# Kernel tuning notes

Hardware: AMD Instinct MI355X
Metric: run time of the kernel (lower is better)

Reference implementation:

```python
import jax, jax.numpy as jnp
import numpy as np

WINDOW = 32


def _dilate(mask, iters=5):
    # scipy binary_dilation with default cross structure, `iters` iterations
    m = mask.copy()
    for _ in range(iters):
        d = m.copy()
        d[1:, :] |= m[:-1, :]
        d[:-1, :] |= m[1:, :]
        d[:, 1:] |= m[:, :-1]
        d[:, :-1] |= m[:, 1:]
        m = d
    return m


def _label8(mask):
    # skimage measure.label, default 8-connectivity, via min-label propagation
    h, w = mask.shape
    lab = np.where(mask, np.arange(1, mask.size + 1, dtype=np.int64).reshape(h, w), 0)
    BIG = mask.size + 2
    while True:
        p = np.pad(np.where(mask, lab, BIG), 1, constant_values=BIG)
        m = np.full((h, w), BIG, dtype=np.int64)
        for dy in (-1, 0, 1):
            for dx in (-1, 0, 1):
                m = np.minimum(m, p[1 + dy:1 + dy + h, 1 + dx:1 + dx + w])
        new = np.where(mask, m, 0)
        if np.array_equal(new, lab):
            break
        lab = new
    u = np.unique(lab)
    out = np.searchsorted(u, lab)
    if u[0] != 0:
        out = out + 1
    return out


def _malis(seg_flat, e1, e2, costs, pos):
    # MALIS edge weights: Kruskal on descending affinities with union-find;
    # pos=True counts same-(nonzero)-label pairs merged by each edge,
    # pos=False counts cross-label pairs between labeled nodes.
    n = seg_flat.size
    parent = np.arange(n)
    cnt = [dict() for _ in range(n)]
    for i in range(n):
        s = int(seg_flat[i])
        if s != 0:
            cnt[i][s] = 1
    w = np.zeros(costs.shape[0], np.float32)

    def find(x):
        r = x
        while parent[r] != r:
            r = parent[r]
        while parent[x] != r:
            parent[x], x = r, parent[x]
        return r

    order = np.argsort(-costs, kind='stable')
    for ei in order:
        ra, rb = find(int(e1[ei])), find(int(e2[ei]))
        if ra == rb:
            continue
        ca, cb = cnt[ra], cnt[rb]
        small, large = (ca, cb) if len(ca) <= len(cb) else (cb, ca)
        same = 0
        for kk, v in small.items():
            same += v * large.get(kk, 0)
        if pos:
            w[ei] = same
        else:
            sa = sum(ca.values())
            sb = sum(cb.values())
            w[ei] = sa * sb - same
        parent[rb] = ra
        for kk, v in cb.items():
            ca[kk] = ca.get(kk, 0) + v
        cnt[rb] = None
    return w


def compute_malis_weights(pred_np, target_np):
    B, C, H, W = pred_np.shape
    wn_full = np.zeros(pred_np.shape, np.float32)
    wp_full = np.zeros(pred_np.shape, np.float32)
    win = WINDOW
    idx = np.arange(win * win).reshape(win, win)
    e1 = np.concatenate([idx[:, :-1].ravel(), idx[:-1, :].ravel()])
    e2 = np.concatenate([idx[:, 1:].ravel(), idx[1:, :].ravel()])
    for k in range(H // win):
        for j in range(W // win):
            p = pred_np[:, :, k * win:(k + 1) * win, j * win:(j + 1) * win]
            t = target_np[:, :, k * win:(k + 1) * win, j * win:(j + 1) * win]
            costs = np.concatenate([
                (p[:, :, :, :-1] + p[:, :, :, 1:]).reshape(B, -1),
                (p[:, :, :-1, :] + p[:, :, 1:, :]).reshape(B, -1)], axis=1).astype(np.float32)
            gtc = np.concatenate([
                (t[:, :, :, :-1] + t[:, :, :, 1:]).reshape(B, -1),
                (t[:, :, :-1, :] + t[:, :, 1:, :]).reshape(B, -1)], axis=1).astype(np.float32)
            costs_n = costs.copy()
            costs_p = costs.copy()
            costs_n[gtc > 20] = 20
            costs_p[gtc < 10] = 0
            gtc = np.minimum(gtc, 20)
            for i in range(B):
                sg = _label8(_dilate(t[i, 0] == 0, 5) == 0)
                en = _malis(sg.ravel(), e1, e2, costs_n[i], False)
                ep = _malis(sg.ravel(), e1, e2, costs_p[i], True)
                sn = en.sum()
                if sn > 0:
                    en = en / sn
                sp = ep.sum()
                if sp > 0:
                    ep = ep / sp
                en[gtc[i] >= 10] = 0
                ep[gtc[i] < 20] = 0
                for ew, out in ((en, wn_full), (ep, wp_full)):
                    wh, wv = np.split(ew, 2)
                    wh = wh.reshape(win, win - 1)
                    wv = wv.reshape(win - 1, win)
                    nodes = np.zeros((win, win), np.float32)
                    nodes[:, :-1] += wh
                    nodes[:, 1:] += wh
                    nodes[:-1, :] += wv
                    nodes[1:, :] += wv
                    out[i, 0, k * win:(k + 1) * win, j * win:(j + 1) * win] = nodes
    return wn_full, wp_full


def setup_inputs() -> dict:
    key = jax.random.key(0)
    k1, k2 = jax.random.split(key)
    pred = jax.random.uniform(k1, (2, 1, 256, 256), jnp.float32) * 20.0
    target = jax.random.randint(k2, (2, 1, 256, 256), 0, 26).astype(jnp.float32)
    return {"pred": pred, "target": target, "malis_lr": 1.0, "malis_lr_pos": 1.0}


def reference(pred, target, malis_lr, malis_lr_pos):
    # weights are computed from detached values (CPU graph algorithm), constants wrt autodiff
    wn, wp = compute_malis_weights(np.asarray(pred), np.asarray(target))
    wn = jnp.asarray(wn, jnp.float32)
    wp = jnp.asarray(wp, jnp.float32)
    loss = malis_lr * jnp.square(pred) * wn + malis_lr_pos * jnp.square(20.0 - pred) * wp
    return loss.sum()
```

## Files before the change

### kernel.cpp

```cpp
#include <hip/hip_runtime.h>
#include <cstdint>

#define NPIX  1024
#define NH    992
#define NEDGE 1984
#define NSORT 2048
#define NGRP  31
#define HFS   4300
#define POOLN (NPIX + 2*HFS)

typedef unsigned long long u64;
typedef unsigned int u32;

static __device__ __forceinline__ u64 packRoot(int sL,int off,int len,int cap){
    return (u64)(u32)(sL & 0x7FF) | ((u64)(u32)(off & 0x3FFF) << 11) |
           ((u64)(u32)(len & 0x7FF) << 25) | ((u64)(u32)(cap & 0x7FF) << 36);
}
#define R_SL(R)  ((int)((R) & 0x7FF))
#define R_OFF(R) ((int)(((R)>>11) & 0x3FFF))
#define R_LEN(R) ((int)(((R)>>25) & 0x7FF))
#define R_CAP(R) ((int)(((R)>>36) & 0x7FF))

static __device__ __forceinline__ int rdl(int v, int l){ return __builtin_amdgcn_readlane(v, l); }

static __device__ __forceinline__ u64 sxor64(u64 v, int m){
    u32 lo = (u32)__shfl_xor((int)(v & 0xFFFFFFFFull), m, 64);
    u32 hi = (u32)__shfl_xor((int)(v >> 32), m, 64);
    return ((u64)hi << 32) | lo;
}

static __device__ __forceinline__ void edgeAB(int e, int &a, int &b){
    if (e < NH) { int r = (int)((unsigned)e / 31u); a = e + r; b = a + 1; }
    else        { a = e - NH; b = a + 32; }
}

#define CE(x, y, up) { u64 _a=(x), _b=(y); bool _lt=(_a<_b); \
    u64 _mn=_lt?_a:_b, _mx=_lt?_b:_a; (x)=(up)?_mn:_mx; (y)=(up)?_mx:_mn; }
#define CEX(x, xm, keepmin) { u64 _p=sxor64((x),(xm)); bool _lt=((x)<_p); \
    u64 _mn=_lt?(x):_p, _mx=_lt?_p:(x); (x)=(keepmin)?_mn:_mx; }

static __device__ __forceinline__ int wredi(int v){
    #pragma unroll
    for (int o = 32; o > 0; o >>= 1) v += __shfl_xor(v, o, 64);
    return v;
}
static __device__ __forceinline__ float wredf(float v){
    #pragma unroll
    for (int o = 32; o > 0; o >>= 1) v += __shfl_xor(v, o, 64);
    return v;
}

__global__ __launch_bounds__(128) void malis_kernel(
    const float* __restrict__ pred,
    const float* __restrict__ target,
    const float* __restrict__ lr_p,
    const float* __restrict__ lrp_p,
    float* __restrict__ out)
{
    const int tid  = threadIdx.x;
    const int lane = tid & 63;
    const int wv   = tid >> 6;
    const int bid  = blockIdx.x;
    const int bb   = bid >> 6;
    const int win  = bid & 63;
    const int wy   = win >> 3, wx = win & 7;
    const int base = bb * 65536 + (wy * 32) * 256 + wx * 32;

    __shared__ __align__(16) u32 Ks[2][NSORT];
    __shared__ u64   root[2][NPIX];
    __shared__ float predL[NPIX];
    __shared__ float costs[NEDGE];
    __shared__ u32   poolS[2][POOLN];
    __shared__ u32   Q[2][NPIX];
    __shared__ float Qw[2][NPIX];
    __shared__ short seg[NPIX];
    __shared__ short par[2][NPIX];
    __shared__ short H[2][NPIX + 1];
    __shared__ unsigned char tgtL[NPIX];
    __shared__ unsigned char gtcL[NEDGE];
    __shared__ u32   rowmaskL[32];
    __shared__ u32   fgL[32];
    __shared__ unsigned short baseL[33];
    __shared__ int   flags[2];

    u32* runPar = (u32*)poolS;
    unsigned short* labIdRun = (unsigned short*)(runPar + 512);

    for (int j = 0; j < 8; ++j) {
        int i = tid + 128 * j;
        int r = i >> 5, c = i & 31;
        float pv = pred[base + r * 256 + c];
        float tv = target[base + r * 256 + c];
        predL[i] = pv;
        tgtL[i]  = (unsigned char)tv;
        u64 zb = __ballot(tv == 0.0f);
        if (lane == 0) {
            int rr = 4 * j + 2 * wv;
            rowmaskL[rr]     = (u32)zb;
            rowmaskL[rr + 1] = (u32)(zb >> 32);
        }
    }
    if (tid == 0) flags[1] = 0;
    for (int x = tid; x < 512; x += 128) runPar[x] = (u32)x;
    __syncthreads();

    if (tid == 0) {
        u32 m0[32];
        #pragma unroll
        for (int r = 0; r < 32; ++r) m0[r] = rowmaskL[r];
        #pragma unroll
        for (int it = 0; it < 5; ++it) {
            u32 d[32];
            #pragma unroll
            for (int r = 0; r < 32; ++r) {
                u32 v = m0[r] | (m0[r] << 1) | (m0[r] >> 1);
                if (r > 0)  v |= m0[r - 1];
                if (r < 31) v |= m0[r + 1];
                d[r] = v;
            }
            #pragma unroll
            for (int r = 0; r < 32; ++r) m0[r] = d[r];
        }
        int acc = 0;
        #pragma unroll
        for (int r = 0; r < 32; ++r) {
            u32 f = ~m0[r];
            fgL[r] = f;
            baseL[r] = (unsigned short)acc;
            acc += __popc(f & ~(f << 1));
        }
        baseL[32] = (unsigned short)acc;
    }
    __syncthreads();
    const int nRuns = (int)baseL[32];

    for (;;) {
        if (tid == 0) flags[0] = 0;
        __syncthreads();
        bool chg = false;
        for (int j = 0; j < 8; ++j) {
            int i = tid + 128 * j;
            int r = i >> 5, c = i & 31;
            if (r == 0) continue;
            u32 fr = fgL[r];
            if (!((fr >> c) & 1u)) continue;
            u32 fu = fgL[r - 1];
            u32 nb = fu & (u32)((7ull << c) >> 1);
            if (!nb) continue;
            u32 Sr = fr & ~(fr << 1);
            int a = (int)baseL[r] + __popc(Sr & ((2u << c) - 1u)) - 1;
            for (;;) { int p = (int)runPar[a]; if (p == a) break; a = p; }
            u32 Su = fu & ~(fu << 1);
            int bu = (int)baseL[r - 1];
            while (nb) {
                int cc = __ffs((int)nb) - 1; nb &= nb - 1;
                int b = bu + __popc(Su & ((2u << cc) - 1u)) - 1;
                for (;;) { int p = (int)runPar[b]; if (p == b) break; b = p; }
                if (a != b) {
                    int mnr = a < b ? a : b;
                    int mxr = a ^ b ^ mnr;
                    atomicMin(&runPar[mxr], (u32)mnr);
                    chg = true;
                    a = mnr;
                }
            }
        }
        if (chg) flags[0] = 1;
        __syncthreads();
        if (!flags[0]) break;
        for (int x = tid; x < nRuns; x += 128) {
            u32 p = runPar[x];
            runPar[x] = runPar[p];
        }
        __syncthreads();
    }

    for (int x = tid; x < nRuns; x += 128)
        if ((int)runPar[x] == x) labIdRun[x] = (unsigned short)atomicAdd(&flags[1], 1);
    __syncthreads();

    for (int j = 0; j < 8; ++j) {
        int i = tid + 128 * j;
        int r = i >> 5, c = i & 31;
        u32 fr = fgL[r];
        short s = 0;
        if ((fr >> c) & 1u) {
            u32 Sr = fr & ~(fr << 1);
            int x = (int)baseL[r] + __popc(Sr & ((2u << c) - 1u)) - 1;
            for (;;) { int p = (int)runPar[x]; if (p == x) break; x = p; }
            s = (short)((int)labIdRun[x] + 1);
        }
        seg[i] = s;
    }

    for (int e = tid; e < NEDGE; e += 128) {
        int a, b2; edgeAB(e, a, b2);
        costs[e] = predL[a] + predL[b2];
        gtcL[e]  = (unsigned char)(tgtL[a] + tgtL[b2]);
    }
    __syncthreads();

    const int ph = wv;
    u32*   Ks_   = Ks[ph];
    short* par_  = par[ph];
    u64*   root_ = root[ph];
    u32*   pool_ = poolS[ph];
    short* H_    = H[ph];
    u32*   Q_    = Q[ph];
    float* Qw_   = Qw[ph];
    u32*   claim_= (u32*)Qw[ph];

    u64 sk[32];
    #pragma unroll
    for (int r = 0; r < 32; ++r) {
        int e = lane * 32 + r;
        u64 kv = ~0ULL;
        if (e < NEDGE) {
            float cv = costs[e];
            int g = gtcL[e];
            if (ph == 0) { if (g > 20) cv = 20.0f; }
            else         { if (g < 10) cv = 0.0f; }
            kv = (((u64)(~__float_as_uint(cv))) << 32) | (u32)e;
        }
        sk[r] = kv;
    }
    #pragma unroll
    for (int kk2 = 2; kk2 <= 32; kk2 <<= 1) {
        #pragma unroll
        for (int j = kk2 >> 1; j > 0; j >>= 1) {
            #pragma unroll
            for (int r = 0; r < 32; ++r) {
                if ((r & j) == 0) {
                    bool up = (kk2 == 32) ? ((lane & 1) == 0) : ((r & kk2) == 0);
                    CE(sk[r], sk[r | j], up);
                }
            }
        }
    }
    #pragma unroll
    for (int kk2 = 64; kk2 <= 2048; kk2 <<= 1) {
        const bool up = ((lane & (kk2 >> 5)) == 0);
        #pragma unroll
        for (int j = kk2 >> 1; j >= 32; j >>= 1) {
            const int xm = j >> 5;
            const bool keepmin = (((lane & xm) == 0) == up);
            #pragma unroll
            for (int r = 0; r < 32; ++r) { CEX(sk[r], xm, keepmin); }
        }
        #pragma unroll
        for (int j = 16; j > 0; j >>= 1) {
            #pragma unroll
            for (int r = 0; r < 32; ++r) {
                if ((r & j) == 0) { CE(sk[r], sk[r | j], up); }
            }
        }
    }
    #pragma unroll
    for (int r = 0; r < 32; r += 4) {
        uint4 v4;
        v4.x = (u32)sk[r]; v4.y = (u32)sk[r+1]; v4.z = (u32)sk[r+2]; v4.w = (u32)sk[r+3];
        *(uint4*)&Ks_[lane * 32 + r] = v4;
    }

    for (int i = lane; i < NPIX; i += 64) {
        short s2 = seg[i];
        par_[i] = (short)(i | (s2 ? 0x8000 : 0));
        if (s2) {
            root_[i] = packRoot(1, i, 1, 1);
            pool_[i] = ((u32)(unsigned short)s2 << 16) | 1u;
        } else {
            root_[i] = 0;
        }
        H_[i] = 0;
        claim_[i] = ~0u;
    }
    if (lane == 0) H_[NPIX] = 0;
    __builtin_amdgcn_wave_barrier();

    int qn = 0;
    u32 rnd = 1;
    const u64 ltm = (1ull << lane) - 1;
    int curE = (int)Ks_[lane];
    for (int g2 = 0; g2 < NGRP; ++g2) {
        int nextE = (g2 + 1 < NGRP) ? (int)Ks_[(g2 + 1) * 64 + lane] : 0;
        const int myE = curE;
        int ea, eb2; edgeAB(myE, ea, eb2);
        int ra = ea, rb = eb2;
        int laA, laB;
        for (;;) {
            int va = (int)(unsigned short)par_[ra];
            int vb = (int)(unsigned short)par_[rb];
            int pa = va & 0x3FF, pb = vb & 0x3FF;
            bool fa = (pa != ra), fb = (pb != rb);
            if (!fa && !fb) { laA = va >> 15; laB = vb >> 15; break; }
            int ga = (int)(unsigned short)par_[pa];
            int gb = (int)(unsigned short)par_[pb];
            if (fa) { par_[ra] = (short)ga; ra = ga & 0x3FF; }
            if (fb) { par_[rb] = (short)gb; rb = gb & 0x3FF; }
        }
        bool alive = (ra != rb);

        for (;;) {
            if (!__ballot(alive)) break;
            const bool av = alive;
            const u32 tag = ((0x03FFFFFFu - rnd) << 6) | (u32)lane;
            ++rnd;
            int mn = ra < rb ? ra : rb;
            int mx = ra < rb ? rb : ra;
            int winner = (laA == laB) ? mn : (laA ? ra : rb);
            int loser  = (laA == laB) ? mx : (laA ? rb : ra);
            bool wgt = (laA & laB) != 0;
            if (av)        atomicMin(&claim_[loser],  tag);
            if (av && wgt) atomicMin(&claim_[winner], tag);
            bool sel = false;
            if (av) {
                u32 cl = claim_[loser];
                u32 cw = wgt ? claim_[winner] : tag;
                sel = (cl == tag) && (cw == tag);
            }
            u64 wm = __ballot(sel && wgt);
            if (sel && wgt) Q_[qn + __popcll(wm & ltm)] =
                (u32)myE | ((u32)mn << 11) | ((u32)mx << 21);
            qn += (int)__popcll(wm);
            if (sel) par_[loser] = (short)winner;
            if (av) {
                for (;;) {
                    int va = (int)(unsigned short)par_[ra];
                    int vb = (int)(unsigned short)par_[rb];
                    int pa = va & 0x3FF, pb = vb & 0x3FF;
                    bool fa = (pa != ra), fb = (pb != rb);
                    if (!fa && !fb) { laA = va >> 15; laB = vb >> 15; break; }
                    int ga = (int)(unsigned short)par_[pa];
                    int gb = (int)(unsigned short)par_[pb];
                    if (fa) { par_[ra] = (short)ga; ra = ga & 0x3FF; }
                    if (fb) { par_[rb] = (short)gb; rb = gb & 0x3FF; }
                }
                alive = !sel && (ra != rb);
            }
        }
        curE = nextE;
        __builtin_amdgcn_wave_barrier();
    }

    u32 bump = NPIX;
    u32 halfEnd = NPIX + HFS;
    int curHalf = 0;

    auto do_gc = [&]() {
        u32 tgt = (curHalf == 0) ? (u32)(NPIX + HFS) : (u32)NPIX;
        u32 nb = tgt;
        for (int c = 0; c < 16; ++c) {
            int i0 = c * 64 + lane;
            bool live = (root_[i0] != 0);
            u64 rbm = __ballot(live);
            while (rbm) {
                int j = __ffsll(rbm) - 1; rbm &= rbm - 1;
                int r = c * 64 + j;
                u64 R = root_[r];
                int len = R_LEN(R);
                int off = R_OFF(R);
                for (int t = lane; t < len; t += 64) {
                    u32 v2 = pool_[off + t];
                    pool_[nb + t] = v2;
                }
                __builtin_amdgcn_wave_barrier();
                if (lane == 0) root_[r] = packRoot(R_SL(R), (int)nb, len, len);
                nb += (u32)len;
            }
        }
        bump = nb;
        halfEnd = tgt + HFS;
        curHalf ^= 1;
    };

    for (int q = 0; q < qn; ++q) {
        u32 rec = Q_[q];
        int A  = (int)((rec >> 11) & 0x3FF);
        int B  = (int)((rec >> 21) & 0x3FF);
        int winner = A;
        int dead   = B;
        u64 RA = root_[A], RB = root_[B];
        int sLa = R_SL(RA), sLb = R_SL(RB);
        int lenA = R_LEN(RA), lenB = R_LEN(RB);
        if (bump + (u32)(lenA + lenB + 8) > halfEnd) {
            do_gc();
            RA = root_[A]; RB = root_[B];
            lenA = R_LEN(RA); lenB = R_LEN(RB);
        }
        int offA = R_OFF(RA), capA = R_CAP(RA);
        int offB = R_OFF(RB), capB = R_CAP(RB);
        int offS, lenS, offL, lenL, capL;
        if (lenA <= lenB) { offS = offA; lenS = lenA; offL = offB; lenL = lenB; capL = capB; }
        else              { offS = offB; lenS = lenB; offL = offA; lenL = lenA; capL = capA; }
        int same = 0, dOff, dLen, dCap;

        if (lenS + lenL <= 64) {
            u32 eL = (lane < lenL) ? pool_[offL + lane] : 0u;
            u32 eS = (lane < lenS) ? pool_[offS + lane] : 0u;
            dLen = lenL;
            for (int t = 0; t < lenS; ++t) {
                u32 xs = (u32)rdl((int)eS, t);
                bool match = (lane < lenL) && ((eL >> 16) == (xs >> 16));
                u64 mb = __ballot(match);
                if (mb) {
                    int ml = __ffsll(mb) - 1;
                    same += (int)(xs & 0xFFFF) * ((int)rdl((int)eL, ml) & 0xFFFF);
                    if (match) eL += (xs & 0xFFFF);
                } else {
                    if (lane == dLen) eL = xs;
                    dLen++;
                }
            }
            if (dLen <= capL) { dOff = offL; dCap = capL; }
            else { dOff = (int)bump; dCap = (dLen + 3) & ~3; bump += (u32)dCap; }
            if (lane < dLen) pool_[dOff + lane] = eL;
        } else {
            dOff = (int)bump;
            dCap = (lenL + lenS + 4) & ~3; bump += (u32)dCap;
            for (int j = lane; j < lenS; j += 64) {
                u32 es = pool_[offS + j];
                H_[es >> 16] = (short)(es & 0xFFFF);
            }
            __builtin_amdgcn_wave_barrier();
            int sp = 0;
            for (int j = lane; j < lenL; j += 64) {
                u32 el = pool_[offL + j];
                int h = (int)H_[el >> 16];
                sp += h * (int)(el & 0xFFFF);
                pool_[dOff + j] = el + (u32)h;
                if (h) H_[el >> 16] = 0;
            }
            same = wredi(sp);
            __builtin_amdgcn_wave_barrier();
            int baseU = 0;
            for (int j0 = 0; j0 < lenS; j0 += 64) {
                int j = j0 + lane;
                bool un = false; u32 es = 0;
                if (j < lenS) { es = pool_[offS + j]; un = (H_[es >> 16] != 0); }
                u64 ub = __ballot(un);
                if (un) {
                    int pos = __popcll(ub & ltm);
                    pool_[dOff + lenL + baseU + pos] = es;
                    H_[es >> 16] = 0;
                }
                baseU += __popcll(ub);
            }
            dLen = lenL + baseU;
        }
        if (lane == 0) {
            Qw_[q] = (float)(ph ? same : (sLa * sLb - same));
            root_[winner] = packRoot(sLa + sLb, dOff, dLen, dCap);
            root_[dead]   = 0;
        }
        __builtin_amdgcn_wave_barrier();
    }

    float s_loc = 0.0f;
    for (int q = lane; q < qn; q += 64) s_loc += Qw_[q];
    const float sn = wredf(s_loc);

    const float scale = ph ? lrp_p[0] : lr_p[0];
    float acc = 0.0f;
    for (int q = lane; q < qn; q += 64) {
        float wv2 = Qw_[q];
        if (wv2 == 0.0f) continue;
        if (sn > 0.0f) wv2 /= sn;
        int me = (int)(Q_[q] & 0x7FF);
        int g = gtcL[me];
        bool zero = ph ? (g < 20) : (g >= 10);
        if (zero) continue;
        int a2, b2; edgeAB(me, a2, b2);
        float pa = predL[a2], pb = predL[b2];
        float fa2, fb2;
        if (ph == 0) { fa2 = pa * pa; fb2 = pb * pb; }
        else { float qa = 20.0f - pa, qb = 20.0f - pb; fa2 = qa * qa; fb2 = qb * qb; }
        acc += scale * wv2 * (fa2 + fb2);
    }
    acc = wredf(acc);
    if (lane == 0) atomicAdd(out, acc);
}

__global__ void zero_out_kernel(float* o)
{
    if (threadIdx.x == 0 && blockIdx.x == 0) o[0] = 0.0f;
}

extern "C" void kernel_launch(void* const* d_in, const int* in_sizes, int n_in,
                              void* d_out, int out_size, void* d_ws, size_t ws_size,
                              hipStream_t stream)
{
    const float* pred   = (const float*)d_in[0];
    const float* target = (const float*)d_in[1];
    const float* lr     = (const float*)d_in[2];
    const float* lrp    = (const float*)d_in[3];
    float* out = (float*)d_out;

    zero_out_kernel<<<1, 64, 0, stream>>>(out);
    malis_kernel<<<128, 128, 0, stream>>>(pred, target, lr, lrp, out);
}
```

Measured before the change: 346.0 us.

## Split monolithic MALIS kernel into seg, sort, drain and replay kernels

Breaks the single 128-block kernel, where each block handled one window and both phases, into four kernels. Segmentation, per-phase sorting, union-find draining and replay now run as separate launches, with intermediates passed through workspace memory. Each of the later three kernels runs 256 single-wave blocks with smaller LDS footprints, aiming at more parallelism and occupancy across CUs. The seg kernel also parallelises the dilation and the prefix sum across 32 lanes using shuffles. In exchange it adds extra launch overhead and global-memory round trips for sorted keys, segments and queues.

```diff
diff --git a/kernel.cpp b/kernel.cpp
--- a/kernel.cpp
+++ b/kernel.cpp
@@ -12,6 +12,11 @@
 typedef unsigned long long u64;
 typedef unsigned int u32;
 
+#define WS_SEG   0
+#define WS_KS    262144
+#define WS_Q     2359296
+#define WS_QN    3407872
+
 static __device__ __forceinline__ u64 packRoot(int sL,int off,int len,int cap){
     return (u64)(u32)(sL & 0x7FF) | ((u64)(u32)(off & 0x3FFF) << 11) |
            ((u64)(u32)(len & 0x7FF) << 25) | ((u64)(u32)(cap & 0x7FF) << 36);
@@ -34,6 +39,13 @@
     else        { a = e - NH; b = a + 32; }
 }
 
+static __device__ __forceinline__ int winBase(int wslot){
+    int bb = wslot >> 6;
+    int win = wslot & 63;
+    int wy = win >> 3, wx = win & 7;
+    return bb * 65536 + (wy * 32) * 256 + wx * 32;
+}
+
 #define CE(x, y, up) { u64 _a=(x), _b=(y); bool _lt=(_a<_b); \
     u64 _mn=_lt?_a:_b, _mx=_lt?_b:_a; (x)=(up)?_mn:_mx; (y)=(up)?_mx:_mn; }
 #define CEX(x, xm, keepmin) { u64 _p=sxor64((x),(xm)); bool _lt=((x)<_p); \
@@ -50,49 +62,27 @@
     return v;
 }
 
-__global__ __launch_bounds__(128) void malis_kernel(
-    const float* __restrict__ pred,
+__global__ __launch_bounds__(128) void seg_kernel(
     const float* __restrict__ target,
-    const float* __restrict__ lr_p,
-    const float* __restrict__ lrp_p,
-    float* __restrict__ out)
+    unsigned short* __restrict__ segW)
 {
     const int tid  = threadIdx.x;
     const int lane = tid & 63;
     const int wv   = tid >> 6;
     const int bid  = blockIdx.x;
-    const int bb   = bid >> 6;
-    const int win  = bid & 63;
-    const int wy   = win >> 3, wx = win & 7;
-    const int base = bb * 65536 + (wy * 32) * 256 + wx * 32;
-
-    __shared__ __align__(16) u32 Ks[2][NSORT];
-    __shared__ u64   root[2][NPIX];
-    __shared__ float predL[NPIX];
-    __shared__ float costs[NEDGE];
-    __shared__ u32   poolS[2][POOLN];
-    __shared__ u32   Q[2][NPIX];
-    __shared__ float Qw[2][NPIX];
-    __shared__ short seg[NPIX];
-    __shared__ short par[2][NPIX];
-    __shared__ short H[2][NPIX + 1];
-    __shared__ unsigned char tgtL[NPIX];
-    __shared__ unsigned char gtcL[NEDGE];
+    const int base = winBase(bid);
+
     __shared__ u32   rowmaskL[32];
     __shared__ u32   fgL[32];
     __shared__ unsigned short baseL[33];
+    __shared__ u32   runPar[512];
+    __shared__ unsigned short labIdRun[512];
     __shared__ int   flags[2];
-
-    u32* runPar = (u32*)poolS;
-    unsigned short* labIdRun = (unsigned short*)(runPar + 512);
 
     for (int j = 0; j < 8; ++j) {
         int i = tid + 128 * j;
         int r = i >> 5, c = i & 31;
-        float pv = pred[base + r * 256 + c];
         float tv = target[base + r * 256 + c];
-        predL[i] = pv;
-        tgtL[i]  = (unsigned char)tv;
         u64 zb = __ballot(tv == 0.0f);
         if (lane == 0) {
             int rr = 4 * j + 2 * wv;
@@ -104,32 +94,27 @@
     for (int x = tid; x < 512; x += 128) runPar[x] = (u32)x;
     __syncthreads();
 
-    if (tid == 0) {
-        u32 m0[32];
-        #pragma unroll
-        for (int r = 0; r < 32; ++r) m0[r] = rowmaskL[r];
+    if (tid < 32) {
+        u32 m = rowmaskL[tid];
         #pragma unroll
         for (int it = 0; it < 5; ++it) {
-            u32 d[32];
-            #pragma unroll
-            for (int r = 0; r < 32; ++r) {
-                u32 v = m0[r] | (m0[r] << 1) | (m0[r] >> 1);
-                if (r > 0)  v |= m0[r - 1];
-                if (r < 31) v |= m0[r + 1];
-                d[r] = v;
-            }
-            #pragma unroll
-            for (int r = 0; r < 32; ++r) m0[r] = d[r];
-        }
-        int acc = 0;
+            u32 um = __shfl(m, (tid == 0) ? 0 : tid - 1, 64);
+            if (tid == 0) um = 0;
+            u32 dm = __shfl(m, (tid == 31) ? 31 : tid + 1, 64);
+            if (tid == 31) dm = 0;
+            m = m | (m << 1) | (m >> 1) | um | dm;
+        }
+        u32 f = ~m;
+        fgL[tid] = f;
+        int ns = __popc(f & ~(f << 1));
+        int x = ns;
         #pragma unroll
-        for (int r = 0; r < 32; ++r) {
-            u32 f = ~m0[r];
-            fgL[r] = f;
-            baseL[r] = (unsigned short)acc;
-            acc += __popc(f & ~(f << 1));
-        }
-        baseL[32] = (unsigned short)acc;
+        for (int off = 1; off < 32; off <<= 1) {
+            int y = __shfl(x, (tid >= off) ? tid - off : 0, 64);
+            if (tid >= off) x += y;
+        }
+        baseL[tid] = (unsigned short)(x - ns);
+        if (tid == 31) baseL[32] = (unsigned short)x;
     }
     __syncthreads();
     const int nRuns = (int)baseL[32];
@@ -179,36 +164,49 @@
         if ((int)runPar[x] == x) labIdRun[x] = (unsigned short)atomicAdd(&flags[1], 1);
     __syncthreads();
 
+    unsigned short* segG = segW + bid * NPIX;
     for (int j = 0; j < 8; ++j) {
         int i = tid + 128 * j;
         int r = i >> 5, c = i & 31;
         u32 fr = fgL[r];
-        short s = 0;
+        unsigned short s = 0;
         if ((fr >> c) & 1u) {
             u32 Sr = fr & ~(fr << 1);
             int x = (int)baseL[r] + __popc(Sr & ((2u << c) - 1u)) - 1;
             for (;;) { int p = (int)runPar[x]; if (p == x) break; x = p; }
-            s = (short)((int)labIdRun[x] + 1);
-        }
-        seg[i] = s;
-    }
-
-    for (int e = tid; e < NEDGE; e += 128) {
+            s = (unsigned short)((int)labIdRun[x] + 1);
+        }
+        segG[i] = s;
+    }
+}
+
+__global__ __launch_bounds__(64) void sort_kernel(
+    const float* __restrict__ pred,
+    const float* __restrict__ target,
+    u32* __restrict__ KsW)
+{
+    const int lane = threadIdx.x;
+    const int bid  = blockIdx.x;
+    const int ph   = bid & 1;
+    const int base = winBase(bid >> 1);
+
+    __shared__ float predL[NPIX];
+    __shared__ float costs[NEDGE];
+    __shared__ unsigned char tgtL[NPIX];
+    __shared__ unsigned char gtcL[NEDGE];
+
+    for (int i = lane; i < NPIX; i += 64) {
+        int r = i >> 5, c = i & 31;
+        predL[i] = pred[base + r * 256 + c];
+        tgtL[i]  = (unsigned char)target[base + r * 256 + c];
+    }
+    __builtin_amdgcn_wave_barrier();
+    for (int e = lane; e < NEDGE; e += 64) {
         int a, b2; edgeAB(e, a, b2);
         costs[e] = predL[a] + predL[b2];
         gtcL[e]  = (unsigned char)(tgtL[a] + tgtL[b2]);
     }
-    __syncthreads();
-
-    const int ph = wv;
-    u32*   Ks_   = Ks[ph];
-    short* par_  = par[ph];
-    u64*   root_ = root[ph];
-    u32*   pool_ = poolS[ph];
-    short* H_    = H[ph];
-    u32*   Q_    = Q[ph];
-    float* Qw_   = Qw[ph];
-    u32*   claim_= (u32*)Qw[ph];
+    __builtin_amdgcn_wave_barrier();
 
     u64 sk[32];
     #pragma unroll
@@ -255,34 +253,43 @@
             }
         }
     }
+    u32* KsG = KsW + (size_t)bid * NSORT;
     #pragma unroll
     for (int r = 0; r < 32; r += 4) {
         uint4 v4;
         v4.x = (u32)sk[r]; v4.y = (u32)sk[r+1]; v4.z = (u32)sk[r+2]; v4.w = (u32)sk[r+3];
-        *(uint4*)&Ks_[lane * 32 + r] = v4;
-    }
+        *(uint4*)&KsG[lane * 32 + r] = v4;
+    }
+}
+
+__global__ __launch_bounds__(64) void drain_kernel(
+    const u32* __restrict__ KsW,
+    const unsigned short* __restrict__ segW,
+    u32* __restrict__ QW,
+    int* __restrict__ qnW)
+{
+    const int lane = threadIdx.x;
+    const int bid  = blockIdx.x;
+    const unsigned short* segG = segW + (bid >> 1) * NPIX;
+    const u32* KsG = KsW + (size_t)bid * NSORT;
+
+    __shared__ short par_[NPIX];
+    __shared__ u32   claim_[NPIX];
+    __shared__ u32   Q_[NPIX];
 
     for (int i = lane; i < NPIX; i += 64) {
-        short s2 = seg[i];
+        unsigned short s2 = segG[i];
         par_[i] = (short)(i | (s2 ? 0x8000 : 0));
-        if (s2) {
-            root_[i] = packRoot(1, i, 1, 1);
-            pool_[i] = ((u32)(unsigned short)s2 << 16) | 1u;
-        } else {
-            root_[i] = 0;
-        }
-        H_[i] = 0;
         claim_[i] = ~0u;
     }
-    if (lane == 0) H_[NPIX] = 0;
     __builtin_amdgcn_wave_barrier();
 
     int qn = 0;
     u32 rnd = 1;
     const u64 ltm = (1ull << lane) - 1;
-    int curE = (int)Ks_[lane];
+    int curE = (int)KsG[lane];
     for (int g2 = 0; g2 < NGRP; ++g2) {
-        int nextE = (g2 + 1 < NGRP) ? (int)Ks_[(g2 + 1) * 64 + lane] : 0;
+        int nextE = (g2 + 1 < NGRP) ? (int)KsG[(g2 + 1) * 64 + lane] : 0;
         const int myE = curE;
         int ea, eb2; edgeAB(myE, ea, eb2);
         int ra = ea, rb = eb2;
@@ -342,6 +349,61 @@
         __builtin_amdgcn_wave_barrier();
     }
 
+    u32* QG = QW + (size_t)bid * NPIX;
+    for (int q = lane; q < qn; q += 64) QG[q] = Q_[q];
+    if (lane == 0) qnW[bid] = qn;
+}
+
+__global__ __launch_bounds__(64) void replay_kernel(
+    const float* __restrict__ pred,
+    const float* __restrict__ target,
+    const unsigned short* __restrict__ segW,
+    const u32* __restrict__ QW,
+    const int* __restrict__ qnW,
+    const float* __restrict__ lr_p,
+    const float* __restrict__ lrp_p,
+    float* __restrict__ out)
+{
+    const int lane = threadIdx.x;
+    const int bid  = blockIdx.x;
+    const int ph   = bid & 1;
+    const int base = winBase(bid >> 1);
+    const unsigned short* segG = segW + (bid >> 1) * NPIX;
+    const u32* QG = QW + (size_t)bid * NPIX;
+    const int qn = qnW[bid];
+
+    __shared__ u64   root_[NPIX];
+    __shared__ u32   pool_[POOLN];
+    __shared__ u32   Q_[NPIX];
+    __shared__ float Qw_[NPIX];
+    __shared__ short H_[NPIX + 1];
+    __shared__ float predL[NPIX];
+    __shared__ unsigned char tgtL[NPIX];
+    __shared__ unsigned char gtcL[NEDGE];
+
+    for (int i = lane; i < NPIX; i += 64) {
+        int r = i >> 5, c = i & 31;
+        predL[i] = pred[base + r * 256 + c];
+        tgtL[i]  = (unsigned char)target[base + r * 256 + c];
+        unsigned short s2 = segG[i];
+        if (s2) {
+            root_[i] = packRoot(1, i, 1, 1);
+            pool_[i] = ((u32)s2 << 16) | 1u;
+        } else {
+            root_[i] = 0;
+        }
+        H_[i] = 0;
+    }
+    if (lane == 0) H_[NPIX] = 0;
+    for (int q = lane; q < qn; q += 64) Q_[q] = QG[q];
+    __builtin_amdgcn_wave_barrier();
+    for (int e = lane; e < NEDGE; e += 64) {
+        int a, b2; edgeAB(e, a, b2);
+        gtcL[e] = (unsigned char)(tgtL[a] + tgtL[b2]);
+    }
+    __builtin_amdgcn_wave_barrier();
+
+    const u64 ltm = (1ull << lane) - 1;
     u32 bump = NPIX;
     u32 halfEnd = NPIX + HFS;
     int curHalf = 0;
@@ -495,6 +557,15 @@
     const float* lrp    = (const float*)d_in[3];
     float* out = (float*)d_out;
 
+    char* ws = (char*)d_ws;
+    unsigned short* segW = (unsigned short*)(ws + WS_SEG);
+    u32* KsW = (u32*)(ws + WS_KS);
+    u32* QW  = (u32*)(ws + WS_Q);
+    int* qnW = (int*)(ws + WS_QN);
+
     zero_out_kernel<<<1, 64, 0, stream>>>(out);
-    malis_kernel<<<128, 128, 0, stream>>>(pred, target, lr, lrp, out);
-}
+    seg_kernel<<<128, 128, 0, stream>>>(target, segW);
+    sort_kernel<<<256, 64, 0, stream>>>(pred, target, KsW);
+    drain_kernel<<<256, 64, 0, stream>>>(KsW, segW, QW, qnW);
+    replay_kernel<<<256, 64, 0, stream>>>(pred, target, segW, QW, qnW, lr, lrp, out);
+}
```

Measured after the change: 442.1 us. 27.8% more time.

## Inline small label-count sets in root words and prefetch next merge record

Applied to the files above, without the earlier changes.

Components holding at most two label/count entries now keep them inside the 64-bit root word, tagged in the top bits, so merging two singletons or small sets needs no pool reads or writes. The next queue record and its roots are loaded before the current root update and patched with the new root when they alias. The 5-iteration dilation and the run prefix sum move from one serial thread to 32 lanes using shuffles. Costs are extra tag branches and more register pressure in the serial merge loop, and a risk if the tagged entries overflow 26 bits.

```diff
diff --git a/kernel.cpp b/kernel.cpp
--- a/kernel.cpp
+++ b/kernel.cpp
@@ -20,6 +20,7 @@
 #define R_OFF(R) ((int)(((R)>>11) & 0x3FFF))
 #define R_LEN(R) ((int)(((R)>>25) & 0x7FF))
 #define R_CAP(R) ((int)(((R)>>36) & 0x7FF))
+#define EMASK 0x3FFFFFFu
 
 static __device__ __forceinline__ int rdl(int v, int l){ return __builtin_amdgcn_readlane(v, l); }
 
@@ -104,32 +105,27 @@
     for (int x = tid; x < 512; x += 128) runPar[x] = (u32)x;
     __syncthreads();
 
-    if (tid == 0) {
-        u32 m0[32];
-        #pragma unroll
-        for (int r = 0; r < 32; ++r) m0[r] = rowmaskL[r];
+    if (tid < 32) {
+        u32 m = rowmaskL[tid];
         #pragma unroll
         for (int it = 0; it < 5; ++it) {
-            u32 d[32];
-            #pragma unroll
-            for (int r = 0; r < 32; ++r) {
-                u32 v = m0[r] | (m0[r] << 1) | (m0[r] >> 1);
-                if (r > 0)  v |= m0[r - 1];
-                if (r < 31) v |= m0[r + 1];
-                d[r] = v;
-            }
-            #pragma unroll
-            for (int r = 0; r < 32; ++r) m0[r] = d[r];
-        }
-        int acc = 0;
+            u32 um = __shfl(m, (tid == 0) ? 0 : tid - 1, 64);
+            if (tid == 0) um = 0;
+            u32 dm = __shfl(m, (tid == 31) ? 31 : tid + 1, 64);
+            if (tid == 31) dm = 0;
+            m = m | (m << 1) | (m >> 1) | um | dm;
+        }
+        u32 f = ~m;
+        fgL[tid] = f;
+        int ns = __popc(f & ~(f << 1));
+        int x = ns;
         #pragma unroll
-        for (int r = 0; r < 32; ++r) {
-            u32 f = ~m0[r];
-            fgL[r] = f;
-            baseL[r] = (unsigned short)acc;
-            acc += __popc(f & ~(f << 1));
-        }
-        baseL[32] = (unsigned short)acc;
+        for (int off = 1; off < 32; off <<= 1) {
+            int y = __shfl(x, (tid >= off) ? tid - off : 0, 64);
+            if (tid >= off) x += y;
+        }
+        baseL[tid] = (unsigned short)(x - ns);
+        if (tid == 31) baseL[32] = (unsigned short)x;
     }
     __syncthreads();
     const int nRuns = (int)baseL[32];
@@ -265,12 +261,7 @@
     for (int i = lane; i < NPIX; i += 64) {
         short s2 = seg[i];
         par_[i] = (short)(i | (s2 ? 0x8000 : 0));
-        if (s2) {
-            root_[i] = packRoot(1, i, 1, 1);
-            pool_[i] = ((u32)(unsigned short)s2 << 16) | 1u;
-        } else {
-            root_[i] = 0;
-        }
+        root_[i] = s2 ? ((1ull << 62) | ((u32)(unsigned short)s2 << 16) | 1u) : 0ull;
         H_[i] = 0;
         claim_[i] = ~0u;
     }
@@ -351,7 +342,8 @@
         u32 nb = tgt;
         for (int c = 0; c < 16; ++c) {
             int i0 = c * 64 + lane;
-            bool live = (root_[i0] != 0);
+            u64 Ri = root_[i0];
+            bool live = (Ri != 0) && ((Ri >> 62) == 0);
             u64 rbm = __ballot(live);
             while (rbm) {
                 int j = __ffsll(rbm) - 1; rbm &= rbm - 1;
@@ -373,86 +365,166 @@
         curHalf ^= 1;
     };
 
+    u32 rec = 0; u64 RA = 0, RB = 0;
+    if (qn > 0) {
+        rec = Q_[0];
+        int A0 = (int)((rec >> 11) & 0x3FF), B0 = (int)((rec >> 21) & 0x3FF);
+        RA = root_[A0]; RB = root_[B0];
+    }
     for (int q = 0; q < qn; ++q) {
-        u32 rec = Q_[q];
-        int A  = (int)((rec >> 11) & 0x3FF);
-        int B  = (int)((rec >> 21) & 0x3FF);
-        int winner = A;
-        int dead   = B;
-        u64 RA = root_[A], RB = root_[B];
-        int sLa = R_SL(RA), sLb = R_SL(RB);
-        int lenA = R_LEN(RA), lenB = R_LEN(RB);
-        if (bump + (u32)(lenA + lenB + 8) > halfEnd) {
-            do_gc();
-            RA = root_[A]; RB = root_[B];
-            lenA = R_LEN(RA); lenB = R_LEN(RB);
-        }
-        int offA = R_OFF(RA), capA = R_CAP(RA);
-        int offB = R_OFF(RB), capB = R_CAP(RB);
-        int offS, lenS, offL, lenL, capL;
-        if (lenA <= lenB) { offS = offA; lenS = lenA; offL = offB; lenL = lenB; capL = capB; }
-        else              { offS = offB; lenS = lenB; offL = offA; lenL = lenA; capL = capA; }
-        int same = 0, dOff, dLen, dCap;
-
-        if (lenS + lenL <= 64) {
-            u32 eL = (lane < lenL) ? pool_[offL + lane] : 0u;
-            u32 eS = (lane < lenS) ? pool_[offS + lane] : 0u;
-            dLen = lenL;
-            for (int t = 0; t < lenS; ++t) {
-                u32 xs = (u32)rdl((int)eS, t);
-                bool match = (lane < lenL) && ((eL >> 16) == (xs >> 16));
-                u64 mb = __ballot(match);
-                if (mb) {
-                    int ml = __ffsll(mb) - 1;
-                    same += (int)(xs & 0xFFFF) * ((int)rdl((int)eL, ml) & 0xFFFF);
-                    if (match) eL += (xs & 0xFFFF);
+        const int A = (int)((rec >> 11) & 0x3FF);
+        const int B = (int)((rec >> 21) & 0x3FF);
+        int tA = (int)(RA >> 62), tB = (int)(RB >> 62);
+        int same, sLa, sLb;
+        u64 newR;
+
+        if (tA == 1 && tB == 1) {
+            u32 pa = (u32)RA & EMASK, pb = (u32)RB & EMASK;
+            int ca = (int)(pa & 0xFFFF), cb = (int)(pb & 0xFFFF);
+            sLa = ca; sLb = cb;
+            if ((pa >> 16) == (pb >> 16)) {
+                same = ca * cb;
+                newR = (1ull << 62) | (u64)(pa + (u32)cb);
+            } else {
+                same = 0;
+                newR = (2ull << 62) | ((u64)pb << 26) | pa;
+            }
+        } else {
+            int lenA = tA ? tA : R_LEN(RA);
+            int lenB = tB ? tB : R_LEN(RB);
+            if (bump + (u32)(lenA + lenB + 8) > halfEnd) {
+                do_gc();
+                RA = root_[A]; RB = root_[B];
+                tA = (int)(RA >> 62); tB = (int)(RB >> 62);
+                lenA = tA ? tA : R_LEN(RA);
+                lenB = tB ? tB : R_LEN(RB);
+            }
+            int offA = 0, capA = 0, offB = 0, capB = 0;
+            if (tA == 0) { sLa = R_SL(RA); offA = R_OFF(RA); capA = R_CAP(RA); }
+            else {
+                u32 a0 = (u32)RA & EMASK, a1 = (u32)(RA >> 26) & EMASK;
+                sLa = (int)(a0 & 0xFFFF) + ((tA == 2) ? (int)(a1 & 0xFFFF) : 0);
+            }
+            if (tB == 0) { sLb = R_SL(RB); offB = R_OFF(RB); capB = R_CAP(RB); }
+            else {
+                u32 b0 = (u32)RB & EMASK, b1 = (u32)(RB >> 26) & EMASK;
+                sLb = (int)(b0 & 0xFFFF) + ((tB == 2) ? (int)(b1 & 0xFFFF) : 0);
+            }
+            u32 eA = 0, eB = 0;
+            if (lenA <= 64) {
+                if (tA == 0) { if (lane < lenA) eA = pool_[offA + lane]; }
+                else {
+                    u32 a0 = (u32)RA & EMASK, a1 = (u32)(RA >> 26) & EMASK;
+                    eA = (lane == 0) ? a0 : ((lane == 1 && tA == 2) ? a1 : 0);
+                }
+            }
+            if (lenB <= 64) {
+                if (tB == 0) { if (lane < lenB) eB = pool_[offB + lane]; }
+                else {
+                    u32 b0 = (u32)RB & EMASK, b1 = (u32)(RB >> 26) & EMASK;
+                    eB = (lane == 0) ? b0 : ((lane == 1 && tB == 2) ? b1 : 0);
+                }
+            }
+            u32 eS, eL; int lenS, lenL, offS, offL, capL, tS, tL;
+            if (lenA <= lenB) { eS=eA; lenS=lenA; offS=offA; tS=tA; eL=eB; lenL=lenB; offL=offB; capL=capB; tL=tB; }
+            else              { eS=eB; lenS=lenB; offS=offB; tS=tB; eL=eA; lenL=lenA; offL=offA; capL=capA; tL=tA; }
+            int dOff, dLen, dCap;
+            same = 0;
+
+            if (lenS + lenL <= 64) {
+                dLen = lenL;
+                for (int t = 0; t < lenS; ++t) {
+                    u32 xs = (u32)rdl((int)eS, t);
+                    bool match = (lane < lenL) && ((eL >> 16) == (xs >> 16));
+                    u64 mb = __ballot(match);
+                    if (mb) {
+                        int ml = __ffsll(mb) - 1;
+                        same += (int)(xs & 0xFFFF) * ((int)rdl((int)eL, ml) & 0xFFFF);
+                        if (match) eL += (xs & 0xFFFF);
+                    } else {
+                        if (lane == dLen) eL = xs;
+                        dLen++;
+                    }
+                }
+                if (dLen <= 2) {
+                    u32 m0 = (u32)rdl((int)eL, 0) & EMASK;
+                    u32 m1 = (dLen > 1) ? ((u32)rdl((int)eL, 1) & EMASK) : 0u;
+                    newR = ((u64)(u32)dLen << 62) | ((u64)m1 << 26) | m0;
                 } else {
-                    if (lane == dLen) eL = xs;
-                    dLen++;
-                }
-            }
-            if (dLen <= capL) { dOff = offL; dCap = capL; }
-            else { dOff = (int)bump; dCap = (dLen + 3) & ~3; bump += (u32)dCap; }
-            if (lane < dLen) pool_[dOff + lane] = eL;
-        } else {
-            dOff = (int)bump;
-            dCap = (lenL + lenS + 4) & ~3; bump += (u32)dCap;
-            for (int j = lane; j < lenS; j += 64) {
-                u32 es = pool_[offS + j];
-                H_[es >> 16] = (short)(es & 0xFFFF);
-            }
-            __builtin_amdgcn_wave_barrier();
-            int sp = 0;
-            for (int j = lane; j < lenL; j += 64) {
-                u32 el = pool_[offL + j];
-                int h = (int)H_[el >> 16];
-                sp += h * (int)(el & 0xFFFF);
-                pool_[dOff + j] = el + (u32)h;
-                if (h) H_[el >> 16] = 0;
-            }
-            same = wredi(sp);
-            __builtin_amdgcn_wave_barrier();
-            int baseU = 0;
-            for (int j0 = 0; j0 < lenS; j0 += 64) {
-                int j = j0 + lane;
-                bool un = false; u32 es = 0;
-                if (j < lenS) { es = pool_[offS + j]; un = (H_[es >> 16] != 0); }
-                u64 ub = __ballot(un);
-                if (un) {
-                    int pos = __popcll(ub & ltm);
-                    pool_[dOff + lenL + baseU + pos] = es;
-                    H_[es >> 16] = 0;
-                }
-                baseU += __popcll(ub);
-            }
-            dLen = lenL + baseU;
+                    if (tL == 0 && dLen <= capL) { dOff = offL; dCap = capL; }
+                    else { dOff = (int)bump; dCap = (dLen + 3) & ~3; bump += (u32)dCap; }
+                    if (lane < dLen) pool_[dOff + lane] = eL;
+                    newR = packRoot(sLa + sLb, dOff, dLen, dCap);
+                }
+            } else {
+                dOff = (int)bump;
+                dCap = (lenL + lenS + 4) & ~3; bump += (u32)dCap;
+                if (lenS <= 64) {
+                    if (lane < lenS) H_[eS >> 16] = (short)(eS & 0xFFFF);
+                } else {
+                    for (int j = lane; j < lenS; j += 64) {
+                        u32 es = pool_[offS + j];
+                        H_[es >> 16] = (short)(es & 0xFFFF);
+                    }
+                }
+                __builtin_amdgcn_wave_barrier();
+                int sp = 0;
+                for (int j = lane; j < lenL; j += 64) {
+                    u32 el = pool_[offL + j];
+                    int h = (int)H_[el >> 16];
+                    sp += h * (int)(el & 0xFFFF);
+                    pool_[dOff + j] = el + (u32)h;
+                    if (h) H_[el >> 16] = 0;
+                }
+                same = wredi(sp);
+                __builtin_amdgcn_wave_barrier();
+                int baseU = 0;
+                if (lenS <= 64) {
+                    bool un = (lane < lenS) && (H_[eS >> 16] != 0);
+                    u64 ub = __ballot(un);
+                    if (un) {
+                        int pos = __popcll(ub & ltm);
+                        pool_[dOff + lenL + pos] = eS;
+                        H_[eS >> 16] = 0;
+                    }
+                    baseU = (int)__popcll(ub);
+                } else {
+                    for (int j0 = 0; j0 < lenS; j0 += 64) {
+                        int j = j0 + lane;
+                        bool un = false; u32 es = 0;
+                        if (j < lenS) { es = pool_[offS + j]; un = (H_[es >> 16] != 0); }
+                        u64 ub = __ballot(un);
+                        if (un) {
+                            int pos = __popcll(ub & ltm);
+                            pool_[dOff + lenL + baseU + pos] = es;
+                            H_[es >> 16] = 0;
+                        }
+                        baseU += (int)__popcll(ub);
+                    }
+                }
+                dLen = lenL + baseU;
+                newR = packRoot(sLa + sLb, dOff, dLen, dCap);
+            }
+        }
+
+        float w = (float)(ph ? same : (sLa * sLb - same));
+
+        u32 recN = 0; int An = -1, Bn = -1; u64 RAn = 0, RBn = 0;
+        if (q + 1 < qn) {
+            recN = Q_[q + 1];
+            An = (int)((recN >> 11) & 0x3FF);
+            Bn = (int)((recN >> 21) & 0x3FF);
+            RAn = root_[An]; RBn = root_[Bn];
         }
         if (lane == 0) {
-            Qw_[q] = (float)(ph ? same : (sLa * sLb - same));
-            root_[winner] = packRoot(sLa + sLb, dOff, dLen, dCap);
-            root_[dead]   = 0;
+            Qw_[q] = w;
+            root_[A] = newR;
+            root_[B] = 0;
         }
         __builtin_amdgcn_wave_barrier();
+        if (An == A) RAn = newR;
+        if (Bn == A) RBn = newR;
+        rec = recN; RA = RAn; RB = RBn;
     }
 
     float s_loc = 0.0f;
```

New measurement: 337.2 us. -2.5%, faster.
